# Performance work log

Hardware: AMD Instinct MI355X
Metric: run time of the kernel (lower is better)

The kernel has to match this reference:

```python
import jax, jax.numpy as jnp
import numpy as np

D_MODEL = 1024
NUM_HEADS = 16
D_K = D_MODEL // NUM_HEADS


def setup_inputs() -> dict:
    key = jax.random.key(0)
    ks = jax.random.split(key, 8)
    B, S = 2, 2048
    query = jax.random.normal(ks[0], (B, S, D_MODEL), dtype=jnp.float32)
    k_in = jax.random.normal(ks[1], (B, S, D_MODEL), dtype=jnp.float32)
    value = jax.random.normal(ks[2], (B, S, D_MODEL), dtype=jnp.float32)
    # causal mask: True = masked out (upper triangle above diagonal)
    mask = jnp.triu(jnp.ones((S, S), dtype=bool), k=1)[None, None, :, :]
    scale = 1.0 / np.sqrt(D_MODEL)
    W_q = jax.random.normal(ks[3], (D_MODEL, D_MODEL), dtype=jnp.float32) * scale
    W_k = jax.random.normal(ks[4], (D_MODEL, D_MODEL), dtype=jnp.float32) * scale
    W_v = jax.random.normal(ks[5], (D_MODEL, D_MODEL), dtype=jnp.float32) * scale
    W_o = jax.random.normal(ks[6], (D_MODEL, D_MODEL), dtype=jnp.float32) * scale
    return {"query": query, "key": k_in, "value": value, "mask": mask,
            "W_q": W_q, "W_k": W_k, "W_v": W_v, "W_o": W_o}


def _split(x):
    # [B, S, d_model] -> [B, h, S, d_k]
    B, S, _ = x.shape
    return x.reshape(B, S, NUM_HEADS, D_K).transpose(0, 2, 1, 3)


def reference(query, key, value, mask, W_q, W_k, W_v, W_o):
    # torch nn.Linear(bias=False): y = x @ W.T
    Q = _split(query @ W_q.T)   # [B, h, Sq, d_k]
    K = _split(key @ W_k.T)     # [B, h, Sk, d_k]
    V = _split(value @ W_v.T)   # [B, h, Sk, d_k]
    scores = jnp.einsum('bhqd,bhkd->bhqk', Q, K) / jnp.sqrt(jnp.float32(D_K))
    scores = jnp.where(mask, -jnp.inf, scores)
    attn_w = jax.nn.softmax(scores, axis=-1)
    attn_w = jnp.nan_to_num(attn_w, nan=0.0)
    out = jnp.einsum('bhqk,bhkd->bhqd', attn_w, V)  # [B, h, Sq, d_k]
    B, _, Sq, _ = out.shape
    merged = out.transpose(0, 2, 1, 3).reshape(B, Sq, D_MODEL)
    return merged @ W_o.T
```

## Files before the change

### kernel.cpp

```cpp
#include <hip/hip_runtime.h>
#include <hip/hip_bf16.h>
#include <stdint.h>

typedef __attribute__((ext_vector_type(4))) float f32x4;
typedef __attribute__((ext_vector_type(8))) __bf16 bf16x8;
typedef __attribute__((ext_vector_type(4))) unsigned short us4;
typedef __attribute__((ext_vector_type(8))) unsigned short us8;

#define SEQ 2048
#define DMODEL 1024
#define NH 16
#define DK 64
#define MTOT 4096

__device__ __forceinline__ unsigned short f2bf(float x) {
  union { float f; unsigned int u; } v; v.f = x;
  unsigned int r = v.u + 0x7fffu + ((v.u >> 16) & 1u);
  return (unsigned short)(r >> 16);
}

__device__ __forceinline__ unsigned int cvtpk(float lo, float hi) {
  unsigned int r;
  asm("v_cvt_pk_bf16_f32 %0, %1, %2" : "=v"(r) : "v"(lo), "v"(hi));
  return r;
}

__device__ __forceinline__ f32x4 mfma_bf16(bf16x8 a, bf16x8 b, f32x4 c) {
  return __builtin_amdgcn_mfma_f32_16x16x32_bf16(a, b, c, 0, 0, 0);
}

__device__ __forceinline__ void gload16(const unsigned short* g, unsigned short* l) {
  __builtin_amdgcn_global_load_lds((__attribute__((address_space(1))) void*)g,
                                   (__attribute__((address_space(3))) void*)l,
                                   16, 0, 0);
}

__global__ void cvt_w(const float* __restrict__ s0, const float* __restrict__ s1,
                      const float* __restrict__ s2, const float* __restrict__ s3,
                      unsigned short* __restrict__ d0, unsigned short* __restrict__ d1,
                      unsigned short* __restrict__ d2, unsigned short* __restrict__ d3) {
  const int y = blockIdx.y;
  const float* s = y == 0 ? s0 : y == 1 ? s1 : y == 2 ? s2 : s3;
  unsigned short* d = y == 0 ? d0 : y == 1 ? d1 : y == 2 ? d2 : d3;
  const int n4 = DMODEL * DMODEL / 4;
  const int stride = gridDim.x * blockDim.x;
  for (int i = blockIdx.x * blockDim.x + threadIdx.x; i < n4; i += stride) {
    f32x4 v = reinterpret_cast<const f32x4*>(s)[i];
    us4 o;
    o.x = f2bf(v.x); o.y = f2bf(v.y); o.z = f2bf(v.z); o.w = f2bf(v.w);
    reinterpret_cast<us4*>(d)[i] = o;
  }
}

__global__ __launch_bounds__(256) void gemm_qk(
    const float* __restrict__ xq, const float* __restrict__ xk,
    const unsigned short* __restrict__ bwq, const unsigned short* __restrict__ bwk,
    unsigned short* __restrict__ Qh, unsigned short* __restrict__ Kh) {
  const int z = blockIdx.z;
  const float* A = z ? xk : xq;
  const unsigned short* B = z ? bwk : bwq;
  unsigned short* out = z ? Kh : Qh;
  const float scale = z ? 1.0f : 0.18033688011112042f;

  __shared__ __align__(16) unsigned short lA[128 * 32];
  __shared__ __align__(16) unsigned short lB[128 * 32];
  const int tid = threadIdx.x;
  const int lane = tid & 63;
  const int wid = tid >> 6;
  const int l15 = lane & 15, l4 = lane >> 4;
  const int bm = blockIdx.x, bn = blockIdx.y;
  const int wr = wid >> 1, wc = wid & 1;

  f32x4 acc[4][4] = {};

  const int chunk0 = (wid * 2 + 0) * 64 + lane;
  const int chunk1 = (wid * 2 + 1) * 64 + lane;
  const float* gAf0 = A + (size_t)(bm * 128 + (chunk0 >> 2)) * 1024 + (chunk0 & 3) * 8;
  const float* gAf1 = A + (size_t)(bm * 128 + (chunk1 >> 2)) * 1024 + (chunk1 & 3) * 8;
  const unsigned short* gB0 = B + (size_t)(bn * 128 + (chunk0 >> 2)) * 1024 + (chunk0 & 3) * 8;
  const unsigned short* gB1 = B + (size_t)(bn * 128 + (chunk1 >> 2)) * 1024 + (chunk1 & 3) * 8;
  unsigned short* wA0 = lA + chunk0 * 8;
  unsigned short* wA1 = lA + chunk1 * 8;
  unsigned short* lB0 = lB + (wid * 2 + 0) * 512;
  unsigned short* lB1 = lB + (wid * 2 + 1) * 512;

  f32x4 ra0 = *reinterpret_cast<const f32x4*>(gAf0);
  f32x4 ra1 = *reinterpret_cast<const f32x4*>(gAf0 + 4);
  f32x4 rb0 = *reinterpret_cast<const f32x4*>(gAf1);
  f32x4 rb1 = *reinterpret_cast<const f32x4*>(gAf1 + 4);

  for (int kt = 0; kt < 1024; kt += 32) {
    __syncthreads();
    union { us8 h; unsigned int u[4]; } p0, p1;
    p0.u[0] = cvtpk(ra0.x, ra0.y); p0.u[1] = cvtpk(ra0.z, ra0.w);
    p0.u[2] = cvtpk(ra1.x, ra1.y); p0.u[3] = cvtpk(ra1.z, ra1.w);
    p1.u[0] = cvtpk(rb0.x, rb0.y); p1.u[1] = cvtpk(rb0.z, rb0.w);
    p1.u[2] = cvtpk(rb1.x, rb1.y); p1.u[3] = cvtpk(rb1.z, rb1.w);
    *reinterpret_cast<us8*>(wA0) = p0.h;
    *reinterpret_cast<us8*>(wA1) = p1.h;
    gload16(gB0 + kt, lB0);
    gload16(gB1 + kt, lB1);
    if (kt + 32 < 1024) {
      ra0 = *reinterpret_cast<const f32x4*>(gAf0 + kt + 32);
      ra1 = *reinterpret_cast<const f32x4*>(gAf0 + kt + 36);
      rb0 = *reinterpret_cast<const f32x4*>(gAf1 + kt + 32);
      rb1 = *reinterpret_cast<const f32x4*>(gAf1 + kt + 36);
    }
    __syncthreads();
    bf16x8 af[4], bfr[4];
#pragma unroll
    for (int i = 0; i < 4; ++i)
      af[i] = *reinterpret_cast<const bf16x8*>(&lA[(wr * 64 + i * 16 + l15) * 32 + l4 * 8]);
#pragma unroll
    for (int j = 0; j < 4; ++j)
      bfr[j] = *reinterpret_cast<const bf16x8*>(&lB[(wc * 64 + j * 16 + l15) * 32 + l4 * 8]);
#pragma unroll
    for (int i = 0; i < 4; ++i)
#pragma unroll
      for (int j = 0; j < 4; ++j)
        acc[i][j] = mfma_bf16(bfr[j], af[i], acc[i][j]);
  }

  const int row0 = bm * 128 + wr * 64;
  const int col0 = bn * 128 + wc * 64;
#pragma unroll
  for (int i = 0; i < 4; ++i) {
    const int m = row0 + i * 16 + l15;
    const int b = m >> 11, s = m & 2047;
#pragma unroll
    for (int j = 0; j < 4; ++j) {
      const int n0 = col0 + j * 16 + l4 * 4;
      const int h = n0 >> 6, dd = n0 & 63;
      union { us4 h4; unsigned int u[2]; } pk;
      pk.u[0] = cvtpk(acc[i][j][0] * scale, acc[i][j][1] * scale);
      pk.u[1] = cvtpk(acc[i][j][2] * scale, acc[i][j][3] * scale);
      *reinterpret_cast<us4*>(&out[(size_t)(b * NH + h) * (SEQ * DK) + s * DK + dd]) = pk.h4;
    }
  }
}

__global__ __launch_bounds__(256) void gemm_v(
    const float* __restrict__ xv, const unsigned short* __restrict__ bwv,
    unsigned short* __restrict__ Vt) {
  __shared__ __align__(16) unsigned short lA[128 * 32];
  __shared__ __align__(16) unsigned short lB[128 * 32];
  const int tid = threadIdx.x;
  const int lane = tid & 63;
  const int wid = tid >> 6;
  const int l15 = lane & 15, l4 = lane >> 4;
  const int bm = blockIdx.x, bn = blockIdx.y;
  const int wr = wid >> 1, wc = wid & 1;

  f32x4 acc[4][4] = {};

  const int chunk0 = (wid * 2 + 0) * 64 + lane;
  const int chunk1 = (wid * 2 + 1) * 64 + lane;
  const float* gAf0 = xv + (size_t)(bm * 128 + (chunk0 >> 2)) * 1024 + (chunk0 & 3) * 8;
  const float* gAf1 = xv + (size_t)(bm * 128 + (chunk1 >> 2)) * 1024 + (chunk1 & 3) * 8;
  const unsigned short* gB0 = bwv + (size_t)(bn * 128 + (chunk0 >> 2)) * 1024 + (chunk0 & 3) * 8;
  const unsigned short* gB1 = bwv + (size_t)(bn * 128 + (chunk1 >> 2)) * 1024 + (chunk1 & 3) * 8;
  unsigned short* wA0 = lA + chunk0 * 8;
  unsigned short* wA1 = lA + chunk1 * 8;
  unsigned short* lB0 = lB + (wid * 2 + 0) * 512;
  unsigned short* lB1 = lB + (wid * 2 + 1) * 512;

  f32x4 ra0 = *reinterpret_cast<const f32x4*>(gAf0);
  f32x4 ra1 = *reinterpret_cast<const f32x4*>(gAf0 + 4);
  f32x4 rb0 = *reinterpret_cast<const f32x4*>(gAf1);
  f32x4 rb1 = *reinterpret_cast<const f32x4*>(gAf1 + 4);

  for (int kt = 0; kt < 1024; kt += 32) {
    __syncthreads();
    union { us8 h; unsigned int u[4]; } p0, p1;
    p0.u[0] = cvtpk(ra0.x, ra0.y); p0.u[1] = cvtpk(ra0.z, ra0.w);
    p0.u[2] = cvtpk(ra1.x, ra1.y); p0.u[3] = cvtpk(ra1.z, ra1.w);
    p1.u[0] = cvtpk(rb0.x, rb0.y); p1.u[1] = cvtpk(rb0.z, rb0.w);
    p1.u[2] = cvtpk(rb1.x, rb1.y); p1.u[3] = cvtpk(rb1.z, rb1.w);
    *reinterpret_cast<us8*>(wA0) = p0.h;
    *reinterpret_cast<us8*>(wA1) = p1.h;
    gload16(gB0 + kt, lB0);
    gload16(gB1 + kt, lB1);
    if (kt + 32 < 1024) {
      ra0 = *reinterpret_cast<const f32x4*>(gAf0 + kt + 32);
      ra1 = *reinterpret_cast<const f32x4*>(gAf0 + kt + 36);
      rb0 = *reinterpret_cast<const f32x4*>(gAf1 + kt + 32);
      rb1 = *reinterpret_cast<const f32x4*>(gAf1 + kt + 36);
    }
    __syncthreads();
    bf16x8 af[4], bfr[4];
#pragma unroll
    for (int i = 0; i < 4; ++i)
      af[i] = *reinterpret_cast<const bf16x8*>(&lA[(wr * 64 + i * 16 + l15) * 32 + l4 * 8]);
#pragma unroll
    for (int j = 0; j < 4; ++j)
      bfr[j] = *reinterpret_cast<const bf16x8*>(&lB[(wc * 64 + j * 16 + l15) * 32 + l4 * 8]);
#pragma unroll
    for (int i = 0; i < 4; ++i)
#pragma unroll
      for (int j = 0; j < 4; ++j)
        acc[i][j] = mfma_bf16(af[i], bfr[j], acc[i][j]);
  }

  const int row0 = bm * 128 + wr * 64;
  const int col0 = bn * 128 + wc * 64;
#pragma unroll
  for (int i = 0; i < 4; ++i) {
    const int m0 = row0 + i * 16 + l4 * 4;
    const int b = m0 >> 11, s0 = m0 & 2047;
    const int g = (s0 >> 2) & 7;
    const int col = (s0 & ~31) + ((g & 3) << 3) + ((g >> 2) << 2);
#pragma unroll
    for (int j = 0; j < 4; ++j) {
      const int n = col0 + j * 16 + l15;
      const int h = n >> 6, dd = n & 63;
      union { us4 h4; unsigned int u[2]; } pk;
      pk.u[0] = cvtpk(acc[i][j][0], acc[i][j][1]);
      pk.u[1] = cvtpk(acc[i][j][2], acc[i][j][3]);
      *reinterpret_cast<us4*>(&Vt[(size_t)(b * NH + h) * (DK * SEQ) + dd * SEQ + col]) = pk.h4;
    }
  }
}

__global__ __launch_bounds__(256) void gemm_o(const unsigned short* __restrict__ A,
                                              const unsigned short* __restrict__ B,
                                              float* __restrict__ out) {
  __shared__ __align__(16) unsigned short lA[128 * 32];
  __shared__ __align__(16) unsigned short lB[128 * 32];
  const int tid = threadIdx.x;
  const int lane = tid & 63;
  const int wid = tid >> 6;
  const int l15 = lane & 15, l4 = lane >> 4;
  const int bm = blockIdx.x, bn = blockIdx.y;
  const int wr = wid >> 1, wc = wid & 1;

  f32x4 acc[4][4] = {};

  const int chunk0 = (wid * 2 + 0) * 64 + lane;
  const int chunk1 = (wid * 2 + 1) * 64 + lane;
  const unsigned short* gA0 = A + (size_t)(bm * 128 + (chunk0 >> 2)) * 1024 + (chunk0 & 3) * 8;
  const unsigned short* gA1 = A + (size_t)(bm * 128 + (chunk1 >> 2)) * 1024 + (chunk1 & 3) * 8;
  const unsigned short* gB0 = B + (size_t)(bn * 128 + (chunk0 >> 2)) * 1024 + (chunk0 & 3) * 8;
  const unsigned short* gB1 = B + (size_t)(bn * 128 + (chunk1 >> 2)) * 1024 + (chunk1 & 3) * 8;
  unsigned short* lA0 = lA + (wid * 2 + 0) * 512;
  unsigned short* lA1 = lA + (wid * 2 + 1) * 512;
  unsigned short* lB0 = lB + (wid * 2 + 0) * 512;
  unsigned short* lB1 = lB + (wid * 2 + 1) * 512;

  for (int kt = 0; kt < 1024; kt += 32) {
    __syncthreads();
    gload16(gA0 + kt, lA0);
    gload16(gA1 + kt, lA1);
    gload16(gB0 + kt, lB0);
    gload16(gB1 + kt, lB1);
    __syncthreads();
    bf16x8 af[4], bfr[4];
#pragma unroll
    for (int i = 0; i < 4; ++i)
      af[i] = *reinterpret_cast<const bf16x8*>(&lA[(wr * 64 + i * 16 + l15) * 32 + l4 * 8]);
#pragma unroll
    for (int j = 0; j < 4; ++j)
      bfr[j] = *reinterpret_cast<const bf16x8*>(&lB[(wc * 64 + j * 16 + l15) * 32 + l4 * 8]);
#pragma unroll
    for (int i = 0; i < 4; ++i)
#pragma unroll
      for (int j = 0; j < 4; ++j)
        acc[i][j] = mfma_bf16(bfr[j], af[i], acc[i][j]);
  }

  const int row0 = bm * 128 + wr * 64;
  const int col0 = bn * 128 + wc * 64;
#pragma unroll
  for (int i = 0; i < 4; ++i) {
    const int m = row0 + i * 16 + l15;
#pragma unroll
    for (int j = 0; j < 4; ++j) {
      const int n0 = col0 + j * 16 + l4 * 4;
      *reinterpret_cast<f32x4*>(&out[(size_t)m * DMODEL + n0]) = acc[i][j];
    }
  }
}

__global__ __launch_bounds__(512, 2) void attn_kernel(const unsigned short* __restrict__ Qh,
                                                      const unsigned short* __restrict__ Kh,
                                                      const unsigned short* __restrict__ Vt,
                                                      unsigned short* __restrict__ Mg) {
  __shared__ __align__(16) unsigned short Kl[4][64 * 64];
  __shared__ __align__(16) unsigned short Vl[4][64 * 64];

  const int tid = threadIdx.x;
  const int lane = tid & 63;
  const int w = tid >> 6;
  const int l15 = lane & 15, l4 = lane >> 4;

  const int d = blockIdx.x;
  const int xcd = d & 7;
  const int j = d >> 3;
  const int bh = (j >> 3) * 8 + xcd;
  const int x = j & 7;

  const unsigned short* Qb = Qh + (size_t)bh * SEQ * DK;
  const unsigned short* Kb = Kh + (size_t)bh * SEQ * DK;
  const unsigned short* Vb = Vt + (size_t)bh * DK * SEQ;
  const int bq = bh >> 4, hh = bh & 15;
  unsigned short* Mbase = Mg + (size_t)bq * SEQ * DMODEL + hh * DK;

  const int srow = lane >> 3;
  const int sswz = (lane & 7) ^ srow;
  const unsigned short* KsrcB = Kb + (size_t)(w * 8 + srow) * DK + sswz * 8;
  const unsigned short* VsrcB = Vb + (size_t)(w * 8 + srow) * SEQ + sswz * 8;

  const int l7 = l15 & 7;

  const int taus[2] = {15 - x, x};

#pragma unroll 1
  for (int seg = 0; seg < 2; ++seg) {
    const int tau = taus[seg];
    const int qbase = tau * 128;
    const int q0w = qbase + w * 16;
    const int nt = 2 * tau + 2;

    __syncthreads();

    bf16x8 qf0 = *reinterpret_cast<const bf16x8*>(Qb + (size_t)(q0w + l15) * DK + l4 * 8);
    bf16x8 qf1 = *reinterpret_cast<const bf16x8*>(Qb + (size_t)(q0w + l15) * DK + 32 + l4 * 8);

    f32x4 o[4] = {};
    float mrow = -__builtin_inff();
    float lrow = 0.0f;

    gload16(KsrcB, &Kl[0][w * 512]);
    gload16(VsrcB, &Vl[0][w * 512]);
    gload16(KsrcB + (size_t)64 * DK, &Kl[1][w * 512]);
    gload16(VsrcB + 64, &Vl[1][w * 512]);

    const int S = nt >> 1;
#pragma unroll 1
    for (int s = 0; s < S; ++s) {
      const int t0 = s << 1;
      const int kbase0 = t0 << 6;

      asm volatile("s_waitcnt vmcnt(0)" ::: "memory");
      __builtin_amdgcn_sched_barrier(0);
      __builtin_amdgcn_s_barrier();
      __builtin_amdgcn_sched_barrier(0);

      if (t0 + 2 < nt) {
        gload16(KsrcB + (size_t)(kbase0 + 128) * DK, &Kl[(t0 + 2) & 3][w * 512]);
        gload16(VsrcB + (kbase0 + 128), &Vl[(t0 + 2) & 3][w * 512]);
        gload16(KsrcB + (size_t)(kbase0 + 192) * DK, &Kl[(t0 + 3) & 3][w * 512]);
        gload16(VsrcB + (kbase0 + 192), &Vl[(t0 + 3) & 3][w * 512]);
      }

#pragma unroll
      for (int u = 0; u < 2; ++u) {
        const int t = t0 + u;
        const int kbase = t << 6;
        if (kbase >= q0w + 16) continue;
        const unsigned short* Kc = Kl[t & 3];
        const unsigned short* Vc = Vl[t & 3];

        f32x4 sc[4];
        __builtin_amdgcn_s_setprio(1);
#pragma unroll
        for (int c = 0; c < 4; ++c) {
          const int krow = c * 16 + l15;
          bf16x8 kf0 = *reinterpret_cast<const bf16x8*>(&Kc[krow * 64 + ((l4 ^ l7) * 8)]);
          bf16x8 kf1 = *reinterpret_cast<const bf16x8*>(&Kc[krow * 64 + (((4 + l4) ^ l7) * 8)]);
          f32x4 z = {0.f, 0.f, 0.f, 0.f};
          z = mfma_bf16(kf0, qf0, z);
          sc[c] = mfma_bf16(kf1, qf1, z);
        }
        __builtin_amdgcn_s_setprio(0);

        if (kbase + 63 > q0w) {
          const int qg = q0w + l15;
#pragma unroll
          for (int c = 0; c < 4; ++c) {
            const int kp = kbase + c * 16 + l4 * 4;
#pragma unroll
            for (int r = 0; r < 4; ++r)
              if (kp + r > qg) sc[c][r] = -__builtin_inff();
          }
        }

        f32x4 mv = sc[0];
#pragma unroll
        for (int c = 1; c < 4; ++c)
#pragma unroll
          for (int r = 0; r < 4; ++r) mv[r] = fmaxf(mv[r], sc[c][r]);
        float pm = fmaxf(fmaxf(mv[0], mv[1]), fmaxf(mv[2], mv[3]));
        if (!__all(pm - mrow <= 8.0f)) {
          pm = fmaxf(pm, __shfl_xor(pm, 16));
          pm = fmaxf(pm, __shfl_xor(pm, 32));
          const float mn = fmaxf(mrow, pm);
          const float al = __builtin_amdgcn_exp2f(mrow - mn);
          mrow = mn;
          lrow *= al;
#pragma unroll
          for (int dd = 0; dd < 4; ++dd)
#pragma unroll
            for (int r = 0; r < 4; ++r) o[dd][r] *= al;
        }
        union PB { bf16x8 v; unsigned int u[4]; } pbv[2];
        f32x4 sv = {0.f, 0.f, 0.f, 0.f};
#pragma unroll
        for (int c = 0; c < 4; ++c) {
          const float p0 = __builtin_amdgcn_exp2f(sc[c][0] - mrow);
          const float p1 = __builtin_amdgcn_exp2f(sc[c][1] - mrow);
          const float p2 = __builtin_amdgcn_exp2f(sc[c][2] - mrow);
          const float p3 = __builtin_amdgcn_exp2f(sc[c][3] - mrow);
          sv[0] += p0; sv[1] += p1; sv[2] += p2; sv[3] += p3;
          pbv[c >> 1].u[(c & 1) * 2 + 0] = cvtpk(p0, p1);
          pbv[c >> 1].u[(c & 1) * 2 + 1] = cvtpk(p2, p3);
        }
        lrow += (sv[0] + sv[1]) + (sv[2] + sv[3]);

        __builtin_amdgcn_s_setprio(1);
#pragma unroll
        for (int dd = 0; dd < 4; ++dd) {
          const int vrow = dd * 16 + l15;
#pragma unroll
          for (int p = 0; p < 2; ++p) {
            const bf16x8 av = *reinterpret_cast<const bf16x8*>(
                &Vc[vrow * 64 + (((p * 4 + l4) ^ l7) * 8)]);
            o[dd] = mfma_bf16(av, pbv[p].v, o[dd]);
          }
        }
        __builtin_amdgcn_s_setprio(0);
      }
    }

    lrow += __shfl_xor(lrow, 16);
    lrow += __shfl_xor(lrow, 32);
    const float inv = __builtin_amdgcn_rcpf(lrow);
    const int s = q0w + l15;
#pragma unroll
    for (int dd = 0; dd < 4; ++dd) {
      union { us4 h; unsigned int u[2]; } pk;
      pk.u[0] = cvtpk(o[dd][0] * inv, o[dd][1] * inv);
      pk.u[1] = cvtpk(o[dd][2] * inv, o[dd][3] * inv);
      *reinterpret_cast<us4*>(&Mbase[(size_t)s * DMODEL + dd * 16 + l4 * 4]) = pk.h;
    }
  }
}

extern "C" void kernel_launch(void* const* d_in, const int* in_sizes, int n_in,
                              void* d_out, int out_size, void* d_ws, size_t ws_size,
                              hipStream_t stream) {
  (void)in_sizes; (void)n_in; (void)out_size;
  if (ws_size < (size_t)64 * (1 << 20)) return;

  const float* q = (const float*)d_in[0];
  const float* k = (const float*)d_in[1];
  const float* v = (const float*)d_in[2];
  const float* wq = (const float*)d_in[4];
  const float* wk = (const float*)d_in[5];
  const float* wv = (const float*)d_in[6];
  const float* wo = (const float*)d_in[7];

  char* ws = (char*)d_ws;
  unsigned short* bwq = (unsigned short*)(ws + (size_t)24 * (1 << 20));
  unsigned short* bwk = (unsigned short*)(ws + (size_t)26 * (1 << 20));
  unsigned short* bwv = (unsigned short*)(ws + (size_t)28 * (1 << 20));
  unsigned short* bwo = (unsigned short*)(ws + (size_t)30 * (1 << 20));
  unsigned short* Qh  = (unsigned short*)(ws + (size_t)32 * (1 << 20));
  unsigned short* Kh  = (unsigned short*)(ws + (size_t)40 * (1 << 20));
  unsigned short* Vt  = (unsigned short*)(ws + (size_t)48 * (1 << 20));
  unsigned short* Mg  = (unsigned short*)(ws + (size_t)56 * (1 << 20));

  cvt_w<<<dim3(64, 4), 256, 0, stream>>>(wq, wk, wv, wo, bwq, bwk, bwv, bwo);
  gemm_qk<<<dim3(32, 8, 2), 256, 0, stream>>>(q, k, bwq, bwk, Qh, Kh);
  gemm_v<<<dim3(32, 8), 256, 0, stream>>>(v, bwv, Vt);
  attn_kernel<<<dim3(256), 512, 0, stream>>>(Qh, Kh, Vt, Mg);
  gemm_o<<<dim3(32, 8), 256, 0, stream>>>(Mg, bwo, (float*)d_out);
}
```

Measured before the change: 127.3 us.

## Merge QKV projections, widen K tile with swizzled LDS, pipeline output GEMM

Merges the Q/K and V projection GEMMs into one launch with a z=3 grid and a 64-wide K tile, and adds an XOR-swizzled LDS layout to avoid bank conflicts. Rewrites the output GEMM to use 512 threads, a triple-buffered LDS pipeline with explicit vmcnt waits and raw barriers, and smaller per-wave tiles. This cuts launch count, halves the number of barrier iterations and overlaps global loads with MFMA work. In exchange it uses more LDS per block, which may lower occupancy.

Measured after the change: 284.6 us. +123.6%, slower.

```diff
diff --git a/kernel.cpp b/kernel.cpp
--- a/kernel.cpp
+++ b/kernel.cpp
@@ -52,225 +52,224 @@
   }
 }
 
-__global__ __launch_bounds__(256) void gemm_qk(
-    const float* __restrict__ xq, const float* __restrict__ xk,
+__global__ __launch_bounds__(256, 3) void gemm_qkv(
+    const float* __restrict__ q, const float* __restrict__ k, const float* __restrict__ v,
     const unsigned short* __restrict__ bwq, const unsigned short* __restrict__ bwk,
-    unsigned short* __restrict__ Qh, unsigned short* __restrict__ Kh) {
+    const unsigned short* __restrict__ bwv,
+    unsigned short* __restrict__ Qh, unsigned short* __restrict__ Kh,
+    unsigned short* __restrict__ Vt) {
   const int z = blockIdx.z;
-  const float* A = z ? xk : xq;
-  const unsigned short* B = z ? bwk : bwq;
-  unsigned short* out = z ? Kh : Qh;
-  const float scale = z ? 1.0f : 0.18033688011112042f;
-
-  __shared__ __align__(16) unsigned short lA[128 * 32];
-  __shared__ __align__(16) unsigned short lB[128 * 32];
+  const float* A = z == 0 ? q : (z == 1 ? k : v);
+  const unsigned short* B = z == 0 ? bwq : (z == 1 ? bwk : bwv);
+  const float scale = z == 0 ? 0.18033688011112042f : 1.0f;
+
+  __shared__ __align__(16) unsigned short lA[128 * 64];
+  __shared__ __align__(16) unsigned short lB[128 * 64];
+
   const int tid = threadIdx.x;
-  const int lane = tid & 63;
-  const int wid = tid >> 6;
+  const int lane = tid & 63, wid = tid >> 6;
   const int l15 = lane & 15, l4 = lane >> 4;
   const int bm = blockIdx.x, bn = blockIdx.y;
   const int wr = wid >> 1, wc = wid & 1;
 
   f32x4 acc[4][4] = {};
 
-  const int chunk0 = (wid * 2 + 0) * 64 + lane;
-  const int chunk1 = (wid * 2 + 1) * 64 + lane;
-  const float* gAf0 = A + (size_t)(bm * 128 + (chunk0 >> 2)) * 1024 + (chunk0 & 3) * 8;
-  const float* gAf1 = A + (size_t)(bm * 128 + (chunk1 >> 2)) * 1024 + (chunk1 & 3) * 8;
-  const unsigned short* gB0 = B + (size_t)(bn * 128 + (chunk0 >> 2)) * 1024 + (chunk0 & 3) * 8;
-  const unsigned short* gB1 = B + (size_t)(bn * 128 + (chunk1 >> 2)) * 1024 + (chunk1 & 3) * 8;
-  unsigned short* wA0 = lA + chunk0 * 8;
-  unsigned short* wA1 = lA + chunk1 * 8;
-  unsigned short* lB0 = lB + (wid * 2 + 0) * 512;
-  unsigned short* lB1 = lB + (wid * 2 + 1) * 512;
-
-  f32x4 ra0 = *reinterpret_cast<const f32x4*>(gAf0);
-  f32x4 ra1 = *reinterpret_cast<const f32x4*>(gAf0 + 4);
-  f32x4 rb0 = *reinterpret_cast<const f32x4*>(gAf1);
-  f32x4 rb1 = *reinterpret_cast<const f32x4*>(gAf1 + 4);
-
-  for (int kt = 0; kt < 1024; kt += 32) {
+  const int arow = tid >> 1, ah = tid & 1;
+  const float* gA = A + (size_t)(bm * 128 + arow) * 1024 + ah * 32;
+  unsigned short* lAr = lA + arow * 64;
+  const int axor = arow & 7;
+
+  const int r8 = lane >> 3, c8 = lane & 7;
+  const unsigned short* gBs[4];
+  unsigned short* lBd[4];
+#pragma unroll
+  for (int is = 0; is < 4; ++is) {
+    const int rbase = is * 32 + wid * 8;
+    gBs[is] = B + (size_t)(bn * 128 + rbase + r8) * 1024 + (c8 ^ r8) * 8;
+    lBd[is] = lB + rbase * 64;
+  }
+
+  f32x4 ar[8];
+#pragma unroll
+  for (int jj = 0; jj < 8; ++jj)
+    ar[jj] = *reinterpret_cast<const f32x4*>(gA + jj * 4);
+
+  for (int kt = 0; kt < 1024; kt += 64) {
     __syncthreads();
-    union { us8 h; unsigned int u[4]; } p0, p1;
-    p0.u[0] = cvtpk(ra0.x, ra0.y); p0.u[1] = cvtpk(ra0.z, ra0.w);
-    p0.u[2] = cvtpk(ra1.x, ra1.y); p0.u[3] = cvtpk(ra1.z, ra1.w);
-    p1.u[0] = cvtpk(rb0.x, rb0.y); p1.u[1] = cvtpk(rb0.z, rb0.w);
-    p1.u[2] = cvtpk(rb1.x, rb1.y); p1.u[3] = cvtpk(rb1.z, rb1.w);
-    *reinterpret_cast<us8*>(wA0) = p0.h;
-    *reinterpret_cast<us8*>(wA1) = p1.h;
-    gload16(gB0 + kt, lB0);
-    gload16(gB1 + kt, lB1);
-    if (kt + 32 < 1024) {
-      ra0 = *reinterpret_cast<const f32x4*>(gAf0 + kt + 32);
-      ra1 = *reinterpret_cast<const f32x4*>(gAf0 + kt + 36);
-      rb0 = *reinterpret_cast<const f32x4*>(gAf1 + kt + 32);
-      rb1 = *reinterpret_cast<const f32x4*>(gAf1 + kt + 36);
-    }
+#pragma unroll
+    for (int j = 0; j < 4; ++j) {
+      union { us8 h; unsigned int u[4]; } pk;
+      pk.u[0] = cvtpk(ar[2 * j][0], ar[2 * j][1]);
+      pk.u[1] = cvtpk(ar[2 * j][2], ar[2 * j][3]);
+      pk.u[2] = cvtpk(ar[2 * j + 1][0], ar[2 * j + 1][1]);
+      pk.u[3] = cvtpk(ar[2 * j + 1][2], ar[2 * j + 1][3]);
+      *reinterpret_cast<us8*>(lAr + (size_t)(((4 * ah + j) ^ axor) * 8)) = pk.h;
+    }
+#pragma unroll
+    for (int is = 0; is < 4; ++is)
+      gload16(gBs[is] + kt, lBd[is]);
     __syncthreads();
-    bf16x8 af[4], bfr[4];
-#pragma unroll
-    for (int i = 0; i < 4; ++i)
-      af[i] = *reinterpret_cast<const bf16x8*>(&lA[(wr * 64 + i * 16 + l15) * 32 + l4 * 8]);
-#pragma unroll
-    for (int j = 0; j < 4; ++j)
-      bfr[j] = *reinterpret_cast<const bf16x8*>(&lB[(wc * 64 + j * 16 + l15) * 32 + l4 * 8]);
-#pragma unroll
-    for (int i = 0; i < 4; ++i)
-#pragma unroll
-      for (int j = 0; j < 4; ++j)
-        acc[i][j] = mfma_bf16(bfr[j], af[i], acc[i][j]);
+
+    if (kt + 64 < 1024) {
+#pragma unroll
+      for (int jj = 0; jj < 8; ++jj)
+        ar[jj] = *reinterpret_cast<const f32x4*>(gA + kt + 64 + jj * 4);
+    }
+
+#pragma unroll
+    for (int kk = 0; kk < 2; ++kk) {
+      bf16x8 af[4], bf[4];
+#pragma unroll
+      for (int i = 0; i < 4; ++i) {
+        const int row = wr * 64 + i * 16 + l15;
+        af[i] = *reinterpret_cast<const bf16x8*>(
+            &lA[row * 64 + (((kk * 4 + l4) ^ (l15 & 7)) * 8)]);
+      }
+#pragma unroll
+      for (int j = 0; j < 4; ++j) {
+        const int row = wc * 64 + j * 16 + l15;
+        bf[j] = *reinterpret_cast<const bf16x8*>(
+            &lB[row * 64 + (((kk * 4 + l4) ^ (l15 & 7)) * 8)]);
+      }
+      if (z < 2) {
+#pragma unroll
+        for (int i = 0; i < 4; ++i)
+#pragma unroll
+          for (int j = 0; j < 4; ++j)
+            acc[i][j] = mfma_bf16(bf[j], af[i], acc[i][j]);
+      } else {
+#pragma unroll
+        for (int i = 0; i < 4; ++i)
+#pragma unroll
+          for (int j = 0; j < 4; ++j)
+            acc[i][j] = mfma_bf16(af[i], bf[j], acc[i][j]);
+      }
+    }
   }
 
   const int row0 = bm * 128 + wr * 64;
   const int col0 = bn * 128 + wc * 64;
-#pragma unroll
-  for (int i = 0; i < 4; ++i) {
-    const int m = row0 + i * 16 + l15;
-    const int b = m >> 11, s = m & 2047;
-#pragma unroll
-    for (int j = 0; j < 4; ++j) {
-      const int n0 = col0 + j * 16 + l4 * 4;
-      const int h = n0 >> 6, dd = n0 & 63;
-      union { us4 h4; unsigned int u[2]; } pk;
-      pk.u[0] = cvtpk(acc[i][j][0] * scale, acc[i][j][1] * scale);
-      pk.u[1] = cvtpk(acc[i][j][2] * scale, acc[i][j][3] * scale);
-      *reinterpret_cast<us4*>(&out[(size_t)(b * NH + h) * (SEQ * DK) + s * DK + dd]) = pk.h4;
-    }
-  }
-}
-
-__global__ __launch_bounds__(256) void gemm_v(
-    const float* __restrict__ xv, const unsigned short* __restrict__ bwv,
-    unsigned short* __restrict__ Vt) {
-  __shared__ __align__(16) unsigned short lA[128 * 32];
-  __shared__ __align__(16) unsigned short lB[128 * 32];
+
+  if (z < 2) {
+    unsigned short* out = z ? Kh : Qh;
+#pragma unroll
+    for (int i = 0; i < 4; ++i) {
+      const int m = row0 + i * 16 + l15;
+      const int b = m >> 11, s = m & 2047;
+#pragma unroll
+      for (int j = 0; j < 4; ++j) {
+        const int n0 = col0 + j * 16 + l4 * 4;
+        const int h = n0 >> 6, dd = n0 & 63;
+        union { us4 h4; unsigned int u[2]; } pk;
+        pk.u[0] = cvtpk(acc[i][j][0] * scale, acc[i][j][1] * scale);
+        pk.u[1] = cvtpk(acc[i][j][2] * scale, acc[i][j][3] * scale);
+        *reinterpret_cast<us4*>(&out[(size_t)(b * NH + h) * (SEQ * DK) + s * DK + dd]) = pk.h4;
+      }
+    }
+  } else {
+#pragma unroll
+    for (int i = 0; i < 4; ++i) {
+      const int m0 = row0 + i * 16 + l4 * 4;
+      const int b = m0 >> 11, s0 = m0 & 2047;
+      const int g = (s0 >> 2) & 7;
+      const int col = (s0 & ~31) + ((g & 3) << 3) + ((g >> 2) << 2);
+#pragma unroll
+      for (int j = 0; j < 4; ++j) {
+        const int n = col0 + j * 16 + l15;
+        const int h = n >> 6, dd = n & 63;
+        union { us4 h4; unsigned int u[2]; } pk;
+        pk.u[0] = cvtpk(acc[i][j][0], acc[i][j][1]);
+        pk.u[1] = cvtpk(acc[i][j][2], acc[i][j][3]);
+        *reinterpret_cast<us4*>(&Vt[(size_t)(b * NH + h) * (DK * SEQ) + dd * SEQ + col]) = pk.h4;
+      }
+    }
+  }
+}
+
+__global__ __launch_bounds__(512) void gemm_o(const unsigned short* __restrict__ A,
+                                              const unsigned short* __restrict__ B,
+                                              float* __restrict__ out) {
+  __shared__ __align__(16) unsigned short lA3[3][128 * 64];
+  __shared__ __align__(16) unsigned short lB3[3][128 * 64];
+
   const int tid = threadIdx.x;
-  const int lane = tid & 63;
-  const int wid = tid >> 6;
+  const int lane = tid & 63, wid = tid >> 6;
   const int l15 = lane & 15, l4 = lane >> 4;
   const int bm = blockIdx.x, bn = blockIdx.y;
   const int wr = wid >> 1, wc = wid & 1;
 
-  f32x4 acc[4][4] = {};
-
-  const int chunk0 = (wid * 2 + 0) * 64 + lane;
-  const int chunk1 = (wid * 2 + 1) * 64 + lane;
-  const float* gAf0 = xv + (size_t)(bm * 128 + (chunk0 >> 2)) * 1024 + (chunk0 & 3) * 8;
-  const float* gAf1 = xv + (size_t)(bm * 128 + (chunk1 >> 2)) * 1024 + (chunk1 & 3) * 8;
-  const unsigned short* gB0 = bwv + (size_t)(bn * 128 + (chunk0 >> 2)) * 1024 + (chunk0 & 3) * 8;
-  const unsigned short* gB1 = bwv + (size_t)(bn * 128 + (chunk1 >> 2)) * 1024 + (chunk1 & 3) * 8;
-  unsigned short* wA0 = lA + chunk0 * 8;
-  unsigned short* wA1 = lA + chunk1 * 8;
-  unsigned short* lB0 = lB + (wid * 2 + 0) * 512;
-  unsigned short* lB1 = lB + (wid * 2 + 1) * 512;
-
-  f32x4 ra0 = *reinterpret_cast<const f32x4*>(gAf0);
-  f32x4 ra1 = *reinterpret_cast<const f32x4*>(gAf0 + 4);
-  f32x4 rb0 = *reinterpret_cast<const f32x4*>(gAf1);
-  f32x4 rb1 = *reinterpret_cast<const f32x4*>(gAf1 + 4);
-
-  for (int kt = 0; kt < 1024; kt += 32) {
-    __syncthreads();
-    union { us8 h; unsigned int u[4]; } p0, p1;
-    p0.u[0] = cvtpk(ra0.x, ra0.y); p0.u[1] = cvtpk(ra0.z, ra0.w);
-    p0.u[2] = cvtpk(ra1.x, ra1.y); p0.u[3] = cvtpk(ra1.z, ra1.w);
-    p1.u[0] = cvtpk(rb0.x, rb0.y); p1.u[1] = cvtpk(rb0.z, rb0.w);
-    p1.u[2] = cvtpk(rb1.x, rb1.y); p1.u[3] = cvtpk(rb1.z, rb1.w);
-    *reinterpret_cast<us8*>(wA0) = p0.h;
-    *reinterpret_cast<us8*>(wA1) = p1.h;
-    gload16(gB0 + kt, lB0);
-    gload16(gB1 + kt, lB1);
-    if (kt + 32 < 1024) {
-      ra0 = *reinterpret_cast<const f32x4*>(gAf0 + kt + 32);
-      ra1 = *reinterpret_cast<const f32x4*>(gAf0 + kt + 36);
-      rb0 = *reinterpret_cast<const f32x4*>(gAf1 + kt + 32);
-      rb1 = *reinterpret_cast<const f32x4*>(gAf1 + kt + 36);
-    }
-    __syncthreads();
-    bf16x8 af[4], bfr[4];
-#pragma unroll
-    for (int i = 0; i < 4; ++i)
-      af[i] = *reinterpret_cast<const bf16x8*>(&lA[(wr * 64 + i * 16 + l15) * 32 + l4 * 8]);
-#pragma unroll
-    for (int j = 0; j < 4; ++j)
-      bfr[j] = *reinterpret_cast<const bf16x8*>(&lB[(wc * 64 + j * 16 + l15) * 32 + l4 * 8]);
-#pragma unroll
-    for (int i = 0; i < 4; ++i)
-#pragma unroll
-      for (int j = 0; j < 4; ++j)
-        acc[i][j] = mfma_bf16(af[i], bfr[j], acc[i][j]);
-  }
-
-  const int row0 = bm * 128 + wr * 64;
+  f32x4 acc[2][4] = {};
+
+  const int r8 = lane >> 3, c8 = lane & 7;
+  const unsigned short* gAs[2];
+  const unsigned short* gBs[2];
+  int dstoff[2];
+#pragma unroll
+  for (int is = 0; is < 2; ++is) {
+    const int rbase = is * 64 + wid * 8;
+    gAs[is] = A + (size_t)(bm * 128 + rbase + r8) * 1024 + (c8 ^ r8) * 8;
+    gBs[is] = B + (size_t)(bn * 128 + rbase + r8) * 1024 + (c8 ^ r8) * 8;
+    dstoff[is] = rbase * 64;
+  }
+
+#define STAGE_O(t, buf)                                         \
+  {                                                             \
+    const int kb = (t) * 64;                                    \
+    gload16(gAs[0] + kb, &lA3[buf][dstoff[0]]);                 \
+    gload16(gAs[1] + kb, &lA3[buf][dstoff[1]]);                 \
+    gload16(gBs[0] + kb, &lB3[buf][dstoff[0]]);                 \
+    gload16(gBs[1] + kb, &lB3[buf][dstoff[1]]);                 \
+  }
+
+  STAGE_O(0, 0);
+  STAGE_O(1, 1);
+
+#pragma unroll 1
+  for (int t = 0; t < 16; ++t) {
+    if (t + 1 < 16) {
+      asm volatile("s_waitcnt vmcnt(4)" ::: "memory");
+    } else {
+      asm volatile("s_waitcnt vmcnt(0)" ::: "memory");
+    }
+    __builtin_amdgcn_sched_barrier(0);
+    __builtin_amdgcn_s_barrier();
+    __builtin_amdgcn_sched_barrier(0);
+
+    if (t + 2 < 16) {
+      const int pb = (t + 2) % 3;
+      STAGE_O(t + 2, pb);
+    }
+
+    const unsigned short* La = lA3[t % 3];
+    const unsigned short* Lb = lB3[t % 3];
+#pragma unroll
+    for (int kk = 0; kk < 2; ++kk) {
+      bf16x8 af[2], bf[4];
+#pragma unroll
+      for (int i = 0; i < 2; ++i) {
+        const int row = wr * 32 + i * 16 + l15;
+        af[i] = *reinterpret_cast<const bf16x8*>(
+            &La[row * 64 + (((kk * 4 + l4) ^ (l15 & 7)) * 8)]);
+      }
+#pragma unroll
+      for (int j = 0; j < 4; ++j) {
+        const int row = wc * 64 + j * 16 + l15;
+        bf[j] = *reinterpret_cast<const bf16x8*>(
+            &Lb[row * 64 + (((kk * 4 + l4) ^ (l15 & 7)) * 8)]);
+      }
+#pragma unroll
+      for (int i = 0; i < 2; ++i)
+#pragma unroll
+        for (int j = 0; j < 4; ++j)
+          acc[i][j] = mfma_bf16(bf[j], af[i], acc[i][j]);
+    }
+  }
+#undef STAGE_O
+
+  const int row0 = bm * 128 + wr * 32;
   const int col0 = bn * 128 + wc * 64;
 #pragma unroll
-  for (int i = 0; i < 4; ++i) {
-    const int m0 = row0 + i * 16 + l4 * 4;
-    const int b = m0 >> 11, s0 = m0 & 2047;
-    const int g = (s0 >> 2) & 7;
-    const int col = (s0 & ~31) + ((g & 3) << 3) + ((g >> 2) << 2);
-#pragma unroll
-    for (int j = 0; j < 4; ++j) {
-      const int n = col0 + j * 16 + l15;
-      const int h = n >> 6, dd = n & 63;
-      union { us4 h4; unsigned int u[2]; } pk;
-      pk.u[0] = cvtpk(acc[i][j][0], acc[i][j][1]);
-      pk.u[1] = cvtpk(acc[i][j][2], acc[i][j][3]);
-      *reinterpret_cast<us4*>(&Vt[(size_t)(b * NH + h) * (DK * SEQ) + dd * SEQ + col]) = pk.h4;
-    }
-  }
-}
-
-__global__ __launch_bounds__(256) void gemm_o(const unsigned short* __restrict__ A,
-                                              const unsigned short* __restrict__ B,
-                                              float* __restrict__ out) {
-  __shared__ __align__(16) unsigned short lA[128 * 32];
-  __shared__ __align__(16) unsigned short lB[128 * 32];
-  const int tid = threadIdx.x;
-  const int lane = tid & 63;
-  const int wid = tid >> 6;
-  const int l15 = lane & 15, l4 = lane >> 4;
-  const int bm = blockIdx.x, bn = blockIdx.y;
-  const int wr = wid >> 1, wc = wid & 1;
-
-  f32x4 acc[4][4] = {};
-
-  const int chunk0 = (wid * 2 + 0) * 64 + lane;
-  const int chunk1 = (wid * 2 + 1) * 64 + lane;
-  const unsigned short* gA0 = A + (size_t)(bm * 128 + (chunk0 >> 2)) * 1024 + (chunk0 & 3) * 8;
-  const unsigned short* gA1 = A + (size_t)(bm * 128 + (chunk1 >> 2)) * 1024 + (chunk1 & 3) * 8;
-  const unsigned short* gB0 = B + (size_t)(bn * 128 + (chunk0 >> 2)) * 1024 + (chunk0 & 3) * 8;
-  const unsigned short* gB1 = B + (size_t)(bn * 128 + (chunk1 >> 2)) * 1024 + (chunk1 & 3) * 8;
-  unsigned short* lA0 = lA + (wid * 2 + 0) * 512;
-  unsigned short* lA1 = lA + (wid * 2 + 1) * 512;
-  unsigned short* lB0 = lB + (wid * 2 + 0) * 512;
-  unsigned short* lB1 = lB + (wid * 2 + 1) * 512;
-
-  for (int kt = 0; kt < 1024; kt += 32) {
-    __syncthreads();
-    gload16(gA0 + kt, lA0);
-    gload16(gA1 + kt, lA1);
-    gload16(gB0 + kt, lB0);
-    gload16(gB1 + kt, lB1);
-    __syncthreads();
-    bf16x8 af[4], bfr[4];
-#pragma unroll
-    for (int i = 0; i < 4; ++i)
-      af[i] = *reinterpret_cast<const bf16x8*>(&lA[(wr * 64 + i * 16 + l15) * 32 + l4 * 8]);
-#pragma unroll
-    for (int j = 0; j < 4; ++j)
-      bfr[j] = *reinterpret_cast<const bf16x8*>(&lB[(wc * 64 + j * 16 + l15) * 32 + l4 * 8]);
-#pragma unroll
-    for (int i = 0; i < 4; ++i)
-#pragma unroll
-      for (int j = 0; j < 4; ++j)
-        acc[i][j] = mfma_bf16(bfr[j], af[i], acc[i][j]);
-  }
-
-  const int row0 = bm * 128 + wr * 64;
-  const int col0 = bn * 128 + wc * 64;
-#pragma unroll
-  for (int i = 0; i < 4; ++i) {
+  for (int i = 0; i < 2; ++i) {
     const int m = row0 + i * 16 + l15;
 #pragma unroll
     for (int j = 0; j < 4; ++j) {
@@ -470,8 +469,7 @@
   unsigned short* Mg  = (unsigned short*)(ws + (size_t)56 * (1 << 20));
 
   cvt_w<<<dim3(64, 4), 256, 0, stream>>>(wq, wk, wv, wo, bwq, bwk, bwv, bwo);
-  gemm_qk<<<dim3(32, 8, 2), 256, 0, stream>>>(q, k, bwq, bwk, Qh, Kh);
-  gemm_v<<<dim3(32, 8), 256, 0, stream>>>(v, bwv, Vt);
+  gemm_qkv<<<dim3(32, 8, 3), 256, 0, stream>>>(q, k, v, bwq, bwk, bwv, Qh, Kh, Vt);
   attn_kernel<<<dim3(256), 512, 0, stream>>>(Qh, Kh, Vt, Mg);
-  gemm_o<<<dim3(32, 8), 256, 0, stream>>>(Mg, bwo, (float*)d_out);
-}
+  gemm_o<<<dim3(32, 8), 512, 0, stream>>>(Mg, bwo, (float*)d_out);
+}
```
